# Kernel tuning notes

Measured on AMD Instinct MI355X. Metric: run time of the kernel, lower is better.

The kernel has to match this reference:

```python
import jax, jax.numpy as jnp
import numpy as np

B = 64        # graphs
N0 = 2048     # nodes per graph
DEG = 16      # avg degree
IN = 128      # input_dim
H = 30        # hcs
NH = 11       # heads
OD = 8        # output_dim[i]
K1, K2, K3 = 1844, 1660, 1494  # ceil(0.9*n) chain


def setup_inputs() -> dict:
    key = jax.random.key(0)
    ks = jax.random.split(key, 32)
    N = B * N0
    E = N * DEG
    x = jax.random.normal(ks[0], (N, IN), jnp.float32)
    g = jnp.repeat(jnp.arange(B, dtype=jnp.int32), N0 * DEG)
    src = g * N0 + jax.random.randint(ks[1], (E,), 0, N0, dtype=jnp.int32)
    dst = g * N0 + jax.random.randint(ks[2], (E,), 0, N0, dtype=jnp.int32)
    edge_index = jnp.stack([src, dst])
    edge_attr = jax.random.uniform(ks[3], (E,), jnp.float32)
    batch = jnp.repeat(jnp.arange(B, dtype=jnp.int32), N0)
    s = 0.05
    def W(k, *shape):
        return jax.random.normal(k, shape, jnp.float32) * s
    return {
        'x': x, 'edge_index': edge_index, 'edge_attr': edge_attr, 'batch': batch,
        'ln_g': jnp.ones((IN,), jnp.float32), 'ln_b': jnp.zeros((IN,), jnp.float32),
        'W_rel1': W(ks[4], IN, H), 'b_rel1': W(ks[5], H), 'W_root1': W(ks[6], IN, H),
        'W_rel2': W(ks[7], H, H), 'b_rel2': W(ks[8], H), 'W_root2': W(ks[9], H, H),
        'W_rel3': W(ks[10], H, H), 'b_rel3': W(ks[11], H), 'W_root3': W(ks[12], H, H),
        'pool_w1': W(ks[13], H), 'pool_w2': W(ks[14], H), 'pool_w3': W(ks[15], H),
        'head_W1': W(ks[16], NH, 2 * H, 8 * H), 'head_b1': W(ks[17], NH, 8 * H),
        'head_W2': W(ks[18], NH, 8 * H, 32 * H), 'head_b2': W(ks[19], NH, 32 * H),
        'head_W3': W(ks[20], NH, 32 * H, OD), 'head_b3': W(ks[21], NH, OD),
    }


def _layernorm(x, g, b):
    m = x.mean(-1, keepdims=True)
    v = ((x - m) ** 2).mean(-1, keepdims=True)
    return (x - m) * jax.lax.rsqrt(v + 1e-5) * g + b


def _gconv(x, src, dst, ew, Wr, br, Ws, N):
    # PyG GraphConv: out = lin_rel(sum_j ew*x_j) + lin_root(x)
    agg = jax.ops.segment_sum(x[src] * ew[:, None], dst, num_segments=N)
    return agg @ Wr + br + x @ Ws


def _topk_pool(x, src, dst, ew, w, n, k):
    # score = tanh(x.w/||w||); keep top-k per graph; gate kept nodes by score
    score = jnp.tanh((x @ w) / jnp.linalg.norm(w)).reshape(B, n)
    vals, idx = jax.lax.top_k(score, k)                      # [B,k]
    xg = x.reshape(B, n, -1)
    xk = jnp.take_along_axis(xg, idx[:, :, None], axis=1) * vals[:, :, None]
    x_new = xk.reshape(B * k, -1)
    newidx = jnp.full((B, n), -1, jnp.int32)
    newidx = newidx.at[jnp.arange(B)[:, None], idx].set(
        jnp.broadcast_to(jnp.arange(k, dtype=jnp.int32), (B, k)))
    g = src // n
    ns = newidx[g, src % n]
    nd = newidx[g, dst % n]
    keep = (ns >= 0) & (nd >= 0)
    src_new = jnp.where(keep, g * k + ns, 0)
    dst_new = jnp.where(keep, g * k + nd, 0)
    ew_new = jnp.where(keep, ew, 0.0)
    return x_new, src_new, dst_new, ew_new


def _readout(x, k):
    xg = x.reshape(B, k, -1)
    return jnp.concatenate([xg.max(axis=1), xg.mean(axis=1)], axis=1)  # [B,2H]


def reference(x, edge_index, edge_attr, batch, ln_g, ln_b,
              W_rel1, b_rel1, W_root1, W_rel2, b_rel2, W_root2,
              W_rel3, b_rel3, W_root3, pool_w1, pool_w2, pool_w3,
              head_W1, head_b1, head_W2, head_b2, head_W3, head_b3):
    src, dst = edge_index[0], edge_index[1]
    ew = edge_attr
    h = _layernorm(x, ln_g, ln_b)

    h = jax.nn.relu(_gconv(h, src, dst, ew, W_rel1, b_rel1, W_root1, B * N0))
    h, src, dst, ew = _topk_pool(h, src, dst, ew, pool_w1, N0, K1)
    x1 = _readout(h, K1)

    h = jax.nn.relu(_gconv(h, src, dst, ew, W_rel2, b_rel2, W_root2, B * K1))
    h, src, dst, ew = _topk_pool(h, src, dst, ew, pool_w2, K1, K2)
    x2 = _readout(h, K2)

    h = jax.nn.relu(_gconv(h, src, dst, ew, W_rel3, b_rel3, W_root3, B * K2))
    h, src, dst, ew = _topk_pool(h, src, dst, ew, pool_w3, K2, K3)
    x3 = _readout(h, K3)

    z = jax.nn.relu(x1 + x2 + x3)                                   # [B,60]
    a = jax.nn.relu(jnp.einsum('bd,hdo->hbo', z, head_W1) + head_b1[:, None, :])
    a = jax.nn.relu(jnp.einsum('hbo,hop->hbp', a, head_W2) + head_b2[:, None, :])
    out = jnp.einsum('hbp,hpq->hbq', a, head_W3) + head_b3[:, None, :]
    return out  # [11, B, 8]
```

## Files before the change

kernel.cpp:

```cpp
#include <hip/hip_runtime.h>
#include <hip/hip_bf16.h>

#define B 64
#define N0 2048
#define DEG 16
#define IN_DIM 128
#define H 30
#define NH 11
#define K1 1844
#define K2 1660
#define K3 1494
#define NTOT (B * N0)
#define ETOT (NTOT * DEG)
#define RSTRIDE 32
#define RT 64
#define ESTRIDE1 32768
#define RSEG 16

__global__ __launch_bounds__(256) void k_prep(
    const float* __restrict__ ln_g, const float* __restrict__ ln_b,
    const float* __restrict__ Wrel1, const float* __restrict__ brel1, const float* __restrict__ Wroot1,
    const float* __restrict__ Wrel2, const float* __restrict__ Wroot2,
    const float* __restrict__ Wrel3, const float* __restrict__ Wroot3,
    float* __restrict__ Wc1, float* __restrict__ S1, float* __restrict__ T1,
    float* __restrict__ Wc2, float* __restrict__ Wc3)
{
    int tid = threadIdx.x;
    for (int i = tid; i < IN_DIM * 60; i += 256) {
        int j = i / 60, c = i - j * 60;
        float w = (c < H) ? Wrel1[j * H + c] : Wroot1[j * H + (c - H)];
        Wc1[i] = w * ln_g[j];
    }
    if (tid < 60) {
        int c = tid;
        float s = 0.f, tt = 0.f;
        for (int j = 0; j < IN_DIM; ++j) {
            float w = (c < H) ? Wrel1[j * H + c] : Wroot1[j * H + (c - H)];
            s += w * ln_g[j];
            tt += w * ln_b[j];
        }
        S1[c] = s;
        T1[c] = (c < H) ? tt : tt + brel1[c - H];
    }
    for (int i = tid; i < H * 60; i += 256) {
        int j = i / 60, c = i - j * 60;
        Wc2[i] = (c < H) ? Wrel2[j * H + c] : Wroot2[j * H + (c - H)];
        Wc3[i] = (c < H) ? Wrel3[j * H + c] : Wroot3[j * H + (c - H)];
    }
}

__global__ __launch_bounds__(256) void k_lnproj(
    const float* __restrict__ x, const float* __restrict__ Wc,
    const float* __restrict__ S, const float* __restrict__ T,
    float* __restrict__ rt)
{
    __shared__ float wlds[IN_DIM * 60];
    for (int i = threadIdx.x; i < IN_DIM * 60 / 4; i += 256)
        ((float4*)wlds)[i] = ((const float4*)Wc)[i];
    __syncthreads();
    int lane = threadIdx.x & 63;
    int wid = __builtin_amdgcn_readfirstlane(threadIdx.x >> 6);
    int c = (lane < 60) ? lane : 59;
    float wreg[IN_DIM];
#pragma unroll
    for (int k = 0; k < IN_DIM; ++k) wreg[k] = wlds[k * 60 + c];
    float Sc = S[c], Tc = T[c];
    int outc = (c < 30) ? c : c + 2;
    int rowbase = (blockIdx.x * 4 + wid) * 64;
    for (int rr = 0; rr < 64; ++rr) {
        int row = rowbase + rr;
        const float4* xr4 = (const float4*)(x + (size_t)row * IN_DIM);
        float xa = x[(size_t)row * IN_DIM + lane];
        float xb = x[(size_t)row * IN_DIM + 64 + lane];
        float s1 = xa + xb;
        float s2 = xa * xa + xb * xb;
#pragma unroll
        for (int off = 32; off > 0; off >>= 1) {
            s1 += __shfl_xor(s1, off, 64);
            s2 += __shfl_xor(s2, off, 64);
        }
        float mean = s1 * (1.f / 128.f);
        float var = s2 * (1.f / 128.f) - mean * mean;
        float rstd = 1.0f / sqrtf(var + 1e-5f);
        float acc0 = 0.f, acc1 = 0.f;
#pragma unroll
        for (int q = 0; q < 32; q += 2) {
            float4 xq0 = xr4[q];
            float4 xq1 = xr4[q + 1];
            acc0 = fmaf(xq0.x, wreg[q * 4 + 0], acc0);
            acc1 = fmaf(xq1.x, wreg[q * 4 + 4], acc1);
            acc0 = fmaf(xq0.y, wreg[q * 4 + 1], acc0);
            acc1 = fmaf(xq1.y, wreg[q * 4 + 5], acc1);
            acc0 = fmaf(xq0.z, wreg[q * 4 + 2], acc0);
            acc1 = fmaf(xq1.z, wreg[q * 4 + 6], acc1);
            acc0 = fmaf(xq0.w, wreg[q * 4 + 3], acc0);
            acc1 = fmaf(xq1.w, wreg[q * 4 + 7], acc1);
        }
        float outv = rstd * ((acc0 + acc1) - mean * Sc) + Tc;
        if (lane < 60)
            rt[(size_t)row * RT + outc] = outv;
    }
}

__global__ __launch_bounds__(256) void k_proj30p(
    const float* __restrict__ hbuf, const int* __restrict__ sidx,
    const float* __restrict__ score, const float* __restrict__ Wc,
    const float* __restrict__ brel, float* __restrict__ rt,
    int n_old, int k)
{
    __shared__ float wlds[4][32][16];
    for (int i = threadIdx.x; i < 30 * 64; i += 256) {
        int m = i >> 6, cc = i & 63;
        int cg = cc >> 4, j = cc & 15;
        wlds[cg][m][j] = (j < 15) ? Wc[m * 60 + cg * 15 + j] : 0.f;
    }
    __syncthreads();
    int lane = threadIdx.x & 63, cg = threadIdx.x >> 6;
    int row0 = blockIdx.x * 256 + lane;
    float acc[4][15];
#pragma unroll
    for (int ri = 0; ri < 4; ++ri)
#pragma unroll
        for (int c = 0; c < 15; ++c) acc[ri][c] = 0.f;
    float vals[4];
    const float* hp[4];
#pragma unroll
    for (int ri = 0; ri < 4; ++ri) {
        int row = row0 + ri * 64;
        int g = row / k, j = row - g * k;
        int idx = sidx[g * k + j];
        vals[ri] = score[g * n_old + idx];
        hp[ri] = hbuf + (size_t)(g * n_old + idx) * RSTRIDE;
    }
    for (int mb = 0; mb < 7; ++mb) {
        float4 cur[4];
#pragma unroll
        for (int ri = 0; ri < 4; ++ri) cur[ri] = *(const float4*)(hp[ri] + mb * 4);
#pragma unroll
        for (int kk = 0; kk < 4; ++kk) {
            int m = mb * 4 + kk;
            float4 w0 = *(const float4*)&wlds[cg][m][0];
            float4 w1 = *(const float4*)&wlds[cg][m][4];
            float4 w2 = *(const float4*)&wlds[cg][m][8];
            float4 w3 = *(const float4*)&wlds[cg][m][12];
#pragma unroll
            for (int ri = 0; ri < 4; ++ri) {
                float xv = (kk == 0) ? cur[ri].x : (kk == 1) ? cur[ri].y
                          : (kk == 2) ? cur[ri].z : cur[ri].w;
                acc[ri][0]  += xv * w0.x; acc[ri][1]  += xv * w0.y;
                acc[ri][2]  += xv * w0.z; acc[ri][3]  += xv * w0.w;
                acc[ri][4]  += xv * w1.x; acc[ri][5]  += xv * w1.y;
                acc[ri][6]  += xv * w1.z; acc[ri][7]  += xv * w1.w;
                acc[ri][8]  += xv * w2.x; acc[ri][9]  += xv * w2.y;
                acc[ri][10] += xv * w2.z; acc[ri][11] += xv * w2.w;
                acc[ri][12] += xv * w3.x; acc[ri][13] += xv * w3.y;
                acc[ri][14] += xv * w3.z;
            }
        }
    }
    {
        float2 h2[4];
#pragma unroll
        for (int ri = 0; ri < 4; ++ri) h2[ri] = *(const float2*)(hp[ri] + 28);
#pragma unroll
        for (int kk = 0; kk < 2; ++kk) {
            int m = 28 + kk;
            float4 w0 = *(const float4*)&wlds[cg][m][0];
            float4 w1 = *(const float4*)&wlds[cg][m][4];
            float4 w2 = *(const float4*)&wlds[cg][m][8];
            float4 w3 = *(const float4*)&wlds[cg][m][12];
#pragma unroll
            for (int ri = 0; ri < 4; ++ri) {
                float xv = (kk == 0) ? h2[ri].x : h2[ri].y;
                acc[ri][0]  += xv * w0.x; acc[ri][1]  += xv * w0.y;
                acc[ri][2]  += xv * w0.z; acc[ri][3]  += xv * w0.w;
                acc[ri][4]  += xv * w1.x; acc[ri][5]  += xv * w1.y;
                acc[ri][6]  += xv * w1.z; acc[ri][7]  += xv * w1.w;
                acc[ri][8]  += xv * w2.x; acc[ri][9]  += xv * w2.y;
                acc[ri][10] += xv * w2.z; acc[ri][11] += xv * w2.w;
                acc[ri][12] += xv * w3.x; acc[ri][13] += xv * w3.y;
                acc[ri][14] += xv * w3.z;
            }
        }
    }
    bool isR = (cg < 2);
    int coff = (isR ? 0 : 32) + (cg & 1) * 15;
    float sB[15];
#pragma unroll
    for (int c = 0; c < 15; ++c) sB[c] = isR ? 0.f : brel[(cg & 1) * 15 + c];
#pragma unroll
    for (int ri = 0; ri < 4; ++ri) {
        int row = row0 + ri * 64;
        float val = vals[ri];
        float* op = rt + (size_t)row * RT + coff;
#pragma unroll
        for (int c = 0; c < 15; ++c)
            op[c] = val * acc[ri][c] + sB[c];
    }
}

__global__ __launch_bounds__(1024) void k_hist1(
    const int* __restrict__ dst, unsigned short* __restrict__ rank,
    int* __restrict__ chunkCnt)
{
    __shared__ unsigned int cnt[2048];
    int chunk = blockIdx.x, g = chunk >> 2;
    for (int i = threadIdx.x; i < 2048; i += 1024) cnt[i] = 0;
    __syncthreads();
    int e0 = chunk * 8192;
#pragma unroll
    for (int u = 0; u < 8; ++u) {
        int e = e0 + u * 1024 + threadIdx.x;
        int d = dst[e] - g * N0;
        rank[e] = (unsigned short)atomicAdd(&cnt[d], 1u);
    }
    __syncthreads();
    for (int i = threadIdx.x; i < 2048; i += 1024) chunkCnt[chunk * 2048 + i] = cnt[i];
}

__global__ __launch_bounds__(1024) void k_scan(
    int* __restrict__ chunkCnt, int* __restrict__ runStart, int* __restrict__ runLen)
{
    __shared__ int bufA[2048], bufB[2048];
    int g = blockIdx.x;
    int c0[2], c1[2], c2[2], tt[2];
    for (int h2 = 0; h2 < 2; ++h2) {
        int d = threadIdx.x + h2 * 1024;
        c0[h2] = chunkCnt[(g * 4 + 0) * 2048 + d];
        c1[h2] = chunkCnt[(g * 4 + 1) * 2048 + d];
        c2[h2] = chunkCnt[(g * 4 + 2) * 2048 + d];
        int c3 = chunkCnt[(g * 4 + 3) * 2048 + d];
        tt[h2] = c0[h2] + c1[h2] + c2[h2] + c3;
        bufA[d] = tt[h2];
    }
    __syncthreads();
    int* s_ = bufA; int* d_ = bufB;
    for (int off = 1; off < 2048; off <<= 1) {
        for (int h2 = 0; h2 < 2; ++h2) {
            int d = threadIdx.x + h2 * 1024;
            int v = s_[d];
            if (d >= off) v += s_[d - off];
            d_[d] = v;
        }
        __syncthreads();
        int* tmp = s_; s_ = d_; d_ = tmp;
    }
    for (int h2 = 0; h2 < 2; ++h2) {
        int d = threadIdx.x + h2 * 1024;
        int ex = s_[d] - tt[h2];
        runStart[g * 2048 + d] = ex;
        runLen[g * 2048 + d] = tt[h2];
        chunkCnt[(g * 4 + 0) * 2048 + d] = ex;
        chunkCnt[(g * 4 + 1) * 2048 + d] = ex + c0[h2];
        chunkCnt[(g * 4 + 2) * 2048 + d] = ex + c0[h2] + c1[h2];
        chunkCnt[(g * 4 + 3) * 2048 + d] = ex + c0[h2] + c1[h2] + c2[h2];
    }
}

__global__ __launch_bounds__(1024) void k_scat1(
    const int* __restrict__ src, const int* __restrict__ dst, const float* __restrict__ ew,
    const unsigned short* __restrict__ rank, const int* __restrict__ chunkOff,
    float2* __restrict__ sOut)
{
    int chunk = blockIdx.x, g = chunk >> 2;
    int e0 = chunk * 8192;
#pragma unroll
    for (int u = 0; u < 8; ++u) {
        int e = e0 + u * 1024 + threadIdx.x;
        int d = dst[e] - g * N0;
        int pos = chunkOff[chunk * 2048 + d] + (int)rank[e];
        sOut[(size_t)g * ESTRIDE1 + pos] = make_float2(__int_as_float(src[e]), ew[e]);
    }
}

template<int LVL>
__global__ __launch_bounds__(256) void k_gather(
    const float2* __restrict__ sE, const int* __restrict__ runS, const int* __restrict__ runL,
    const int* __restrict__ ind1, const int* __restrict__ ind2, const int* __restrict__ mapc,
    const float* __restrict__ rt, float* __restrict__ h,
    const float* __restrict__ poolw, float* __restrict__ score,
    int n, int rK, int nblocks)
{
    int b = blockIdx.x;
    int cpx = nblocks >> 3;
    b = (b & 7) * cpx + (b >> 3);
    int slot = threadIdx.x >> 5, j = threadIdx.x & 31;
    int v = b * 8 + slot;
    int g = v / n;
    int local = v - g * n;
    int v1 = local;
    if (LVL >= 2) v1 = ind2[g * K2 + v1];
    if (LVL >= 1) v1 = ind1[g * K1 + v1];
    int s0 = runS[g * 2048 + v1], len = runL[g * 2048 + v1];
    const float2* meta = sE + (size_t)g * ESTRIDE1 + s0;
    int rbase = g * rK;
    float acc = 0.f;
    for (int c = 0; c < len; c += 8) {
        int lim = len - c; if (lim > 8) lim = 8;
        float2 m[8];
#pragma unroll
        for (int u = 0; u < 8; ++u) m[u] = meta[c + (u < lim ? u : 0)];
        int rowv[8]; float wv[8];
#pragma unroll
        for (int u = 0; u < 8; ++u) {
            int srcg = __float_as_int(m[u].x);
            float w = (u < lim) ? m[u].y : 0.f;
            if (LVL == 0) {
                rowv[u] = srcg;
            } else {
                int ss = mapc[srcg];
                rowv[u] = rbase + (ss < 0 ? 0 : ss);
                w = (ss < 0) ? 0.f : w;
            }
            wv[u] = w;
        }
#pragma unroll
        for (int u = 0; u < 8; ++u)
            acc += rt[(size_t)rowv[u] * RT + j] * wv[u];
    }
    float wj = (j < H) ? poolw[j] : 0.f;
    float hval = 0.f;
    if (j < H) {
        hval = fmaxf(acc + rt[(size_t)v * RT + 32 + j], 0.f);
        h[(size_t)v * RSTRIDE + j] = hval;
    }
    float p = hval * wj, q = wj * wj;
#pragma unroll
    for (int off = 16; off > 0; off >>= 1) {
        p += __shfl_xor(p, off, 32);
        q += __shfl_xor(q, off, 32);
    }
    if (j == 0) score[v] = tanhf(p / sqrtf(q));
}

__global__ __launch_bounds__(1024) void k_topk_map(
    const float* __restrict__ score, int* __restrict__ sidx, int* __restrict__ mapc,
    int n, int k, int first)
{
    __shared__ unsigned long long keys[2048];
    __shared__ int inv[2048];
    int g = blockIdx.x;
    for (int i = threadIdx.x; i < 2048; i += 1024) {
        unsigned long long key = ~0ull;
        if (i < n) {
            float s = score[g * n + i];
            if (s == 0.f) s = 0.f;
            unsigned u = __float_as_uint(s);
            unsigned asc = (u & 0x80000000u) ? ~u : (u | 0x80000000u);
            unsigned desc = ~asc;
            key = ((unsigned long long)desc << 32) | (unsigned)i;
        }
        keys[i] = key;
        inv[i] = -1;
    }
    __syncthreads();
    for (int kk = 2; kk <= 2048; kk <<= 1) {
        for (int jj = kk >> 1; jj > 0; jj >>= 1) {
            for (int i = threadIdx.x; i < 2048; i += 1024) {
                int ixj = i ^ jj;
                if (ixj > i) {
                    unsigned long long a = keys[i], bb = keys[ixj];
                    bool up = ((i & kk) == 0);
                    if ((a > bb) == up) { keys[i] = bb; keys[ixj] = a; }
                }
            }
            __syncthreads();
        }
    }
    for (int j = threadIdx.x; j < k; j += 1024) {
        int idx = (int)(keys[j] & 0xffffffffu);
        sidx[g * k + j] = idx;
        inv[idx] = j;
    }
    __syncthreads();
    if (first) {
        for (int v = threadIdx.x; v < N0; v += 1024)
            mapc[g * N0 + v] = inv[v];
    } else {
        for (int v = threadIdx.x; v < N0; v += 1024) {
            int m = mapc[g * N0 + v];
            mapc[g * N0 + v] = (m >= 0) ? inv[m] : -1;
        }
    }
}

__global__ __launch_bounds__(256) void k_rpart(
    const float* __restrict__ hbuf, const int* __restrict__ sidx,
    const float* __restrict__ score, float* __restrict__ pmax, float* __restrict__ psum,
    int n_old, int k)
{
    __shared__ float smax[8][32], ssum[8][32];
    int g = blockIdx.y, seg = blockIdx.x;
    int clen = (k + RSEG - 1) / RSEG;
    int start = seg * clen;
    int end = start + clen; if (end > k) end = k;
    int f = threadIdx.x & 31, rr = threadIdx.x >> 5;
    float mx = -INFINITY, sm = 0.f;
    if (f < H) {
        for (int j = start + rr; j < end; j += 8) {
            int idx = sidx[g * k + j];
            float val = score[g * n_old + idx];
            float v = hbuf[(size_t)(g * n_old + idx) * RSTRIDE + f] * val;
            mx = fmaxf(mx, v);
            sm += v;
        }
    }
    smax[rr][f] = mx; ssum[rr][f] = sm;
    __syncthreads();
    if (rr == 0) {
        for (int q = 1; q < 8; ++q) { mx = fmaxf(mx, smax[q][f]); sm += ssum[q][f]; }
        pmax[(g * RSEG + seg) * 32 + f] = mx;
        psum[(g * RSEG + seg) * 32 + f] = sm;
    }
}

__global__ __launch_bounds__(64) void k_zfin(
    const float* __restrict__ pm1, const float* __restrict__ ps1,
    const float* __restrict__ pm2, const float* __restrict__ ps2,
    const float* __restrict__ pm3, const float* __restrict__ ps3,
    float* __restrict__ z)
{
    int g = blockIdx.x, c = threadIdx.x;
    if (c >= 60) return;
    float v1, v2, v3;
    if (c < H) {
        float m1 = -INFINITY, m2 = -INFINITY, m3 = -INFINITY;
        for (int s = 0; s < RSEG; ++s) {
            m1 = fmaxf(m1, pm1[(g * RSEG + s) * 32 + c]);
            m2 = fmaxf(m2, pm2[(g * RSEG + s) * 32 + c]);
            m3 = fmaxf(m3, pm3[(g * RSEG + s) * 32 + c]);
        }
        v1 = m1; v2 = m2; v3 = m3;
    } else {
        int f = c - H;
        float s1 = 0.f, s2 = 0.f, s3 = 0.f;
        for (int s = 0; s < RSEG; ++s) {
            s1 += ps1[(g * RSEG + s) * 32 + f];
            s2 += ps2[(g * RSEG + s) * 32 + f];
            s3 += ps3[(g * RSEG + s) * 32 + f];
        }
        v1 = s1 / (float)K1; v2 = s2 / (float)K2; v3 = s3 / (float)K3;
    }
    z[g * 60 + c] = fmaxf(v1 + v2 + v3, 0.f);
}

__global__ __launch_bounds__(256) void k_mlp1(
    const float* __restrict__ z, const float* __restrict__ W,
    const float* __restrict__ bias, float* __restrict__ a)
{
    int hb = blockIdx.x, hh = hb >> 6, b = hb & 63;
    __shared__ float zr[60];
    if (threadIdx.x < 60) zr[threadIdx.x] = z[b * 60 + threadIdx.x];
    __syncthreads();
    int o = threadIdx.x;
    if (o < 240) {
        float acc = bias[hh * 240 + o];
        const float* Wp = W + hh * 60 * 240;
#pragma unroll
        for (int d = 0; d < 60; ++d) acc += zr[d] * Wp[d * 240 + o];
        a[(hh * B + b) * 240 + o] = fmaxf(acc, 0.f);
    }
}

__global__ __launch_bounds__(256) void k_mlp2(
    const float* __restrict__ a1, const float* __restrict__ W,
    const float* __restrict__ bias, float* __restrict__ a2)
{
    __shared__ float a1t[64 * 240];
    int hh = blockIdx.x / 15, ct = blockIdx.x % 15;
    const float4* ag = (const float4*)(a1 + (size_t)hh * B * 240);
    for (int i = threadIdx.x; i < 64 * 240 / 4; i += 256)
        ((float4*)a1t)[i] = ag[i];
    __syncthreads();
    int col = threadIdx.x & 63, rg = threadIdx.x >> 6;
    const float* Wp = W + (size_t)hh * 240 * 960 + ct * 64 + col;
    float acc[16];
#pragma unroll
    for (int i = 0; i < 16; ++i) acc[i] = 0.f;
#pragma unroll 4
    for (int o = 0; o < 240; ++o) {
        float w = Wp[(size_t)o * 960];
        const float* ar = &a1t[0];
#pragma unroll
        for (int i = 0; i < 16; ++i)
            acc[i] += w * ar[(rg * 16 + i) * 240 + o];
    }
    float bv = bias[hh * 960 + ct * 64 + col];
#pragma unroll
    for (int i = 0; i < 16; ++i)
        a2[((size_t)hh * B + rg * 16 + i) * 960 + ct * 64 + col] =
            fmaxf(acc[i] + bv, 0.f);
}

__global__ __launch_bounds__(64) void k_mlp3(
    const float* __restrict__ a2, const float* __restrict__ W,
    const float* __restrict__ bias, float* __restrict__ out)
{
    int hb = blockIdx.x, hh = hb >> 6, b = hb & 63;
    __shared__ float ar[960];
    __shared__ float part[64];
    for (int i = threadIdx.x; i < 960; i += 64) ar[i] = a2[(hh * B + b) * 960 + i];
    __syncthreads();
    int q = threadIdx.x & 7, c = threadIdx.x >> 3;
    const float* Wp = W + hh * 960 * 8;
    float acc = 0.f;
    for (int p = c; p < 960; p += 8) acc += ar[p] * Wp[p * 8 + q];
    part[threadIdx.x] = acc;
    __syncthreads();
    if (threadIdx.x < 8) {
        float s = bias[hh * 8 + threadIdx.x];
        for (int cc = 0; cc < 8; ++cc) s += part[cc * 8 + threadIdx.x];
        out[(hh * B + b) * 8 + threadIdx.x] = s;
    }
}

extern "C" void kernel_launch(void* const* d_in, const int* in_sizes, int n_in,
                              void* d_out, int out_size, void* d_ws, size_t ws_size,
                              hipStream_t stream)
{
    const float* x       = (const float*)d_in[0];
    const int*   eidx    = (const int*)d_in[1];
    const int*   src0    = eidx;
    const int*   dst0    = eidx + ETOT;
    const float* ew0     = (const float*)d_in[2];
    const float* ln_g    = (const float*)d_in[4];
    const float* ln_b    = (const float*)d_in[5];
    const float* W_rel1  = (const float*)d_in[6];
    const float* b_rel1  = (const float*)d_in[7];
    const float* W_root1 = (const float*)d_in[8];
    const float* W_rel2  = (const float*)d_in[9];
    const float* b_rel2  = (const float*)d_in[10];
    const float* W_root2 = (const float*)d_in[11];
    const float* W_rel3  = (const float*)d_in[12];
    const float* b_rel3  = (const float*)d_in[13];
    const float* W_root3 = (const float*)d_in[14];
    const float* pool_w1 = (const float*)d_in[15];
    const float* pool_w2 = (const float*)d_in[16];
    const float* pool_w3 = (const float*)d_in[17];
    const float* head_W1 = (const float*)d_in[18];
    const float* head_b1 = (const float*)d_in[19];
    const float* head_W2 = (const float*)d_in[20];
    const float* head_b2 = (const float*)d_in[21];
    const float* head_W3 = (const float*)d_in[22];
    const float* head_b3 = (const float*)d_in[23];

    float* ws     = (float*)d_ws;
    float* rtbuf  = ws;
    float* abuf   = rtbuf + (size_t)NTOT * RT;
    float2* sA    = (float2*)(abuf + (size_t)NTOT * RSTRIDE);
    float* score  = (float*)(sA + (size_t)B * ESTRIDE1);
    int*   sidxA  = (int*)(score + NTOT);
    int*   sidxB  = sidxA + B * K1;
    int*   sidxC  = sidxB + B * K2;
    int*   mapc   = sidxC + B * K3;
    int*   runSA  = mapc + NTOT;
    int*   runLA  = runSA + B * 2048;
    float* pm1    = (float*)(runLA + B * 2048);
    float* ps1    = pm1 + B * RSEG * 32;
    float* pm2    = ps1 + B * RSEG * 32;
    float* ps2    = pm2 + B * RSEG * 32;
    float* pm3    = ps2 + B * RSEG * 32;
    float* ps3    = pm3 + B * RSEG * 32;
    float* zb     = ps3 + B * RSEG * 32;
    float* Wc1    = zb + B * 60;
    float* S1     = Wc1 + IN_DIM * 60;
    float* T1     = S1 + 60;
    float* Wc2    = T1 + 60;
    float* Wc3    = Wc2 + H * 60;
    int* chunkBuf         = (int*)abuf;
    unsigned short* rank  = (unsigned short*)((char*)abuf + (4u << 20));
    float* a1 = rtbuf;
    float* a2 = a1 + NH * B * 240;

    k_prep<<<1, 256, 0, stream>>>(ln_g, ln_b, W_rel1, b_rel1, W_root1,
                                  W_rel2, W_root2, W_rel3, W_root3,
                                  Wc1, S1, T1, Wc2, Wc3);

    k_hist1<<<256, 1024, 0, stream>>>(dst0, rank, chunkBuf);
    k_scan<<<B, 1024, 0, stream>>>(chunkBuf, runSA, runLA);
    k_scat1<<<256, 1024, 0, stream>>>(src0, dst0, ew0, rank, chunkBuf, sA);

    k_lnproj<<<NTOT / 256, 256, 0, stream>>>(x, Wc1, S1, T1, rtbuf);
    k_gather<0><<<NTOT / 8, 256, 0, stream>>>(sA, runSA, runLA, nullptr, nullptr, nullptr,
                                              rtbuf, abuf, pool_w1, score,
                                              N0, N0, NTOT / 8);
    k_topk_map<<<B, 1024, 0, stream>>>(score, sidxA, mapc, N0, K1, 1);
    k_rpart<<<dim3(RSEG, B), 256, 0, stream>>>(abuf, sidxA, score, pm1, ps1, N0, K1);
    k_proj30p<<<B * K1 / 256, 256, 0, stream>>>(abuf, sidxA, score, Wc2, b_rel2,
                                                rtbuf, N0, K1);

    k_gather<1><<<B * K1 / 8, 256, 0, stream>>>(sA, runSA, runLA, sidxA, nullptr, mapc,
                                                rtbuf, abuf, pool_w2, score,
                                                K1, K1, B * K1 / 8);
    k_topk_map<<<B, 1024, 0, stream>>>(score, sidxB, mapc, K1, K2, 0);
    k_rpart<<<dim3(RSEG, B), 256, 0, stream>>>(abuf, sidxB, score, pm2, ps2, K1, K2);
    k_proj30p<<<B * K2 / 256, 256, 0, stream>>>(abuf, sidxB, score, Wc3, b_rel3,
                                                rtbuf, K1, K2);

    k_gather<2><<<B * K2 / 8, 256, 0, stream>>>(sA, runSA, runLA, sidxA, sidxB, mapc,
                                                rtbuf, abuf, pool_w3, score,
                                                K2, K2, B * K2 / 8);
    k_topk_map<<<B, 1024, 0, stream>>>(score, sidxC, mapc, K2, K3, 0);
    k_rpart<<<dim3(RSEG, B), 256, 0, stream>>>(abuf, sidxC, score, pm3, ps3, K2, K3);

    k_zfin<<<B, 64, 0, stream>>>(pm1, ps1, pm2, ps2, pm3, ps3, zb);
    k_mlp1<<<NH * B, 256, 0, stream>>>(zb, head_W1, head_b1, a1);
    k_mlp2<<<NH * 15, 256, 0, stream>>>(a1, head_W2, head_b2, a2);
    k_mlp3<<<NH * B, 64, 0, stream>>>(a2, head_W3, head_b3, (float*)d_out);
}
```

Measured before the change: 568.0 us.

## Remap projection kernels to thread-per-row with column groups on grid y

Rewrites k_lnproj and k_proj30p so that each thread computes one row for a 15-column group, with the group chosen by blockIdx.y. Weights are read directly from global memory with uniform addresses instead of being staged in LDS or held in 128 registers per lane. The goal is to cut register and LDS pressure and raise occupancy. The cost is that each input row is now read four times, and the per-thread row reads are strided rather than coalesced across a wave.

Result: slower. 674.0 us (+18.7%).

```diff
diff --git a/kernel.cpp b/kernel.cpp
--- a/kernel.cpp
+++ b/kernel.cpp
@@ -54,52 +54,35 @@
     const float* __restrict__ S, const float* __restrict__ T,
     float* __restrict__ rt)
 {
-    __shared__ float wlds[IN_DIM * 60];
-    for (int i = threadIdx.x; i < IN_DIM * 60 / 4; i += 256)
-        ((float4*)wlds)[i] = ((const float4*)Wc)[i];
-    __syncthreads();
-    int lane = threadIdx.x & 63;
-    int wid = __builtin_amdgcn_readfirstlane(threadIdx.x >> 6);
-    int c = (lane < 60) ? lane : 59;
-    float wreg[IN_DIM];
-#pragma unroll
-    for (int k = 0; k < IN_DIM; ++k) wreg[k] = wlds[k * 60 + c];
-    float Sc = S[c], Tc = T[c];
-    int outc = (c < 30) ? c : c + 2;
-    int rowbase = (blockIdx.x * 4 + wid) * 64;
-    for (int rr = 0; rr < 64; ++rr) {
-        int row = rowbase + rr;
-        const float4* xr4 = (const float4*)(x + (size_t)row * IN_DIM);
-        float xa = x[(size_t)row * IN_DIM + lane];
-        float xb = x[(size_t)row * IN_DIM + 64 + lane];
-        float s1 = xa + xb;
-        float s2 = xa * xa + xb * xb;
-#pragma unroll
-        for (int off = 32; off > 0; off >>= 1) {
-            s1 += __shfl_xor(s1, off, 64);
-            s2 += __shfl_xor(s2, off, 64);
-        }
-        float mean = s1 * (1.f / 128.f);
-        float var = s2 * (1.f / 128.f) - mean * mean;
-        float rstd = 1.0f / sqrtf(var + 1e-5f);
-        float acc0 = 0.f, acc1 = 0.f;
-#pragma unroll
-        for (int q = 0; q < 32; q += 2) {
-            float4 xq0 = xr4[q];
-            float4 xq1 = xr4[q + 1];
-            acc0 = fmaf(xq0.x, wreg[q * 4 + 0], acc0);
-            acc1 = fmaf(xq1.x, wreg[q * 4 + 4], acc1);
-            acc0 = fmaf(xq0.y, wreg[q * 4 + 1], acc0);
-            acc1 = fmaf(xq1.y, wreg[q * 4 + 5], acc1);
-            acc0 = fmaf(xq0.z, wreg[q * 4 + 2], acc0);
-            acc1 = fmaf(xq1.z, wreg[q * 4 + 6], acc1);
-            acc0 = fmaf(xq0.w, wreg[q * 4 + 3], acc0);
-            acc1 = fmaf(xq1.w, wreg[q * 4 + 7], acc1);
-        }
-        float outv = rstd * ((acc0 + acc1) - mean * Sc) + Tc;
-        if (lane < 60)
-            rt[(size_t)row * RT + outc] = outv;
-    }
+    int cg = blockIdx.y;
+    int row = blockIdx.x * 256 + threadIdx.x;
+    const float4* xr4 = (const float4*)(x + (size_t)row * IN_DIM);
+    const float* wbase = Wc + cg * 15;
+    float acc[15];
+#pragma unroll
+    for (int c = 0; c < 15; ++c) acc[c] = 0.f;
+    float sum = 0.f, sumsq = 0.f;
+    for (int k4 = 0; k4 < 32; ++k4) {
+        float4 xq = xr4[k4];
+        float xs[4] = {xq.x, xq.y, xq.z, xq.w};
+#pragma unroll
+        for (int u = 0; u < 4; ++u) {
+            float xv = xs[u];
+            sum += xv; sumsq += xv * xv;
+            const float* wrow = wbase + (k4 * 4 + u) * 60;
+#pragma unroll
+            for (int c = 0; c < 15; ++c) acc[c] += xv * wrow[c];
+        }
+    }
+    float mean = sum * (1.f / 128.f);
+    float var = sumsq * (1.f / 128.f) - mean * mean;
+    float rstd = 1.0f / sqrtf(var + 1e-5f);
+    int scol = cg * 15;
+    int coff = (cg < 2) ? cg * 15 : 32 + (cg - 2) * 15;
+    float* op = rt + (size_t)row * RT + coff;
+#pragma unroll
+    for (int c = 0; c < 15; ++c)
+        op[c] = rstd * (acc[c] - mean * S[scol + c]) + T[scol + c];
 }
 
 __global__ __launch_bounds__(256) void k_proj30p(
@@ -108,94 +91,44 @@
     const float* __restrict__ brel, float* __restrict__ rt,
     int n_old, int k)
 {
-    __shared__ float wlds[4][32][16];
-    for (int i = threadIdx.x; i < 30 * 64; i += 256) {
-        int m = i >> 6, cc = i & 63;
-        int cg = cc >> 4, j = cc & 15;
-        wlds[cg][m][j] = (j < 15) ? Wc[m * 60 + cg * 15 + j] : 0.f;
-    }
-    __syncthreads();
-    int lane = threadIdx.x & 63, cg = threadIdx.x >> 6;
-    int row0 = blockIdx.x * 256 + lane;
-    float acc[4][15];
-#pragma unroll
-    for (int ri = 0; ri < 4; ++ri)
-#pragma unroll
-        for (int c = 0; c < 15; ++c) acc[ri][c] = 0.f;
-    float vals[4];
-    const float* hp[4];
-#pragma unroll
-    for (int ri = 0; ri < 4; ++ri) {
-        int row = row0 + ri * 64;
-        int g = row / k, j = row - g * k;
-        int idx = sidx[g * k + j];
-        vals[ri] = score[g * n_old + idx];
-        hp[ri] = hbuf + (size_t)(g * n_old + idx) * RSTRIDE;
-    }
-    for (int mb = 0; mb < 7; ++mb) {
-        float4 cur[4];
-#pragma unroll
-        for (int ri = 0; ri < 4; ++ri) cur[ri] = *(const float4*)(hp[ri] + mb * 4);
-#pragma unroll
-        for (int kk = 0; kk < 4; ++kk) {
-            int m = mb * 4 + kk;
-            float4 w0 = *(const float4*)&wlds[cg][m][0];
-            float4 w1 = *(const float4*)&wlds[cg][m][4];
-            float4 w2 = *(const float4*)&wlds[cg][m][8];
-            float4 w3 = *(const float4*)&wlds[cg][m][12];
-#pragma unroll
-            for (int ri = 0; ri < 4; ++ri) {
-                float xv = (kk == 0) ? cur[ri].x : (kk == 1) ? cur[ri].y
-                          : (kk == 2) ? cur[ri].z : cur[ri].w;
-                acc[ri][0]  += xv * w0.x; acc[ri][1]  += xv * w0.y;
-                acc[ri][2]  += xv * w0.z; acc[ri][3]  += xv * w0.w;
-                acc[ri][4]  += xv * w1.x; acc[ri][5]  += xv * w1.y;
-                acc[ri][6]  += xv * w1.z; acc[ri][7]  += xv * w1.w;
-                acc[ri][8]  += xv * w2.x; acc[ri][9]  += xv * w2.y;
-                acc[ri][10] += xv * w2.z; acc[ri][11] += xv * w2.w;
-                acc[ri][12] += xv * w3.x; acc[ri][13] += xv * w3.y;
-                acc[ri][14] += xv * w3.z;
-            }
+    int cg = blockIdx.y;
+    int row = blockIdx.x * 256 + threadIdx.x;
+    int g = row / k, j = row - g * k;
+    int idx = sidx[g * k + j];
+    float val = score[g * n_old + idx];
+    const float* hr = hbuf + (size_t)(g * n_old + idx) * RSTRIDE;
+    const float4* hr4 = (const float4*)hr;
+    const float* wbase = Wc + cg * 15;
+    float acc[15];
+#pragma unroll
+    for (int c = 0; c < 15; ++c) acc[c] = 0.f;
+#pragma unroll
+    for (int m4 = 0; m4 < 7; ++m4) {
+        float4 hq = hr4[m4];
+        float xs[4] = {hq.x, hq.y, hq.z, hq.w};
+#pragma unroll
+        for (int u = 0; u < 4; ++u) {
+            float xv = xs[u];
+            const float* wrow = wbase + (m4 * 4 + u) * 60;
+#pragma unroll
+            for (int c = 0; c < 15; ++c) acc[c] += xv * wrow[c];
         }
     }
     {
-        float2 h2[4];
-#pragma unroll
-        for (int ri = 0; ri < 4; ++ri) h2[ri] = *(const float2*)(hp[ri] + 28);
-#pragma unroll
-        for (int kk = 0; kk < 2; ++kk) {
-            int m = 28 + kk;
-            float4 w0 = *(const float4*)&wlds[cg][m][0];
-            float4 w1 = *(const float4*)&wlds[cg][m][4];
-            float4 w2 = *(const float4*)&wlds[cg][m][8];
-            float4 w3 = *(const float4*)&wlds[cg][m][12];
-#pragma unroll
-            for (int ri = 0; ri < 4; ++ri) {
-                float xv = (kk == 0) ? h2[ri].x : h2[ri].y;
-                acc[ri][0]  += xv * w0.x; acc[ri][1]  += xv * w0.y;
-                acc[ri][2]  += xv * w0.z; acc[ri][3]  += xv * w0.w;
-                acc[ri][4]  += xv * w1.x; acc[ri][5]  += xv * w1.y;
-                acc[ri][6]  += xv * w1.z; acc[ri][7]  += xv * w1.w;
-                acc[ri][8]  += xv * w2.x; acc[ri][9]  += xv * w2.y;
-                acc[ri][10] += xv * w2.z; acc[ri][11] += xv * w2.w;
-                acc[ri][12] += xv * w3.x; acc[ri][13] += xv * w3.y;
-                acc[ri][14] += xv * w3.z;
-            }
-        }
+        float2 h2 = *(const float2*)(hr + 28);
+        const float* w28 = wbase + 28 * 60;
+        const float* w29 = wbase + 29 * 60;
+#pragma unroll
+        for (int c = 0; c < 15; ++c)
+            acc[c] += h2.x * w28[c] + h2.y * w29[c];
     }
     bool isR = (cg < 2);
-    int coff = (isR ? 0 : 32) + (cg & 1) * 15;
-    float sB[15];
-#pragma unroll
-    for (int c = 0; c < 15; ++c) sB[c] = isR ? 0.f : brel[(cg & 1) * 15 + c];
-#pragma unroll
-    for (int ri = 0; ri < 4; ++ri) {
-        int row = row0 + ri * 64;
-        float val = vals[ri];
-        float* op = rt + (size_t)row * RT + coff;
-#pragma unroll
-        for (int c = 0; c < 15; ++c)
-            op[c] = val * acc[ri][c] + sB[c];
+    int coff = isR ? cg * 15 : 32 + (cg - 2) * 15;
+    float* op = rt + (size_t)row * RT + coff;
+#pragma unroll
+    for (int c = 0; c < 15; ++c) {
+        float bv = isR ? 0.f : brel[(cg - 2) * 15 + c];
+        op[c] = val * acc[c] + bv;
     }
 }
 
@@ -580,22 +513,22 @@
     k_scan<<<B, 1024, 0, stream>>>(chunkBuf, runSA, runLA);
     k_scat1<<<256, 1024, 0, stream>>>(src0, dst0, ew0, rank, chunkBuf, sA);
 
-    k_lnproj<<<NTOT / 256, 256, 0, stream>>>(x, Wc1, S1, T1, rtbuf);
+    k_lnproj<<<dim3(NTOT / 256, 4), 256, 0, stream>>>(x, Wc1, S1, T1, rtbuf);
     k_gather<0><<<NTOT / 8, 256, 0, stream>>>(sA, runSA, runLA, nullptr, nullptr, nullptr,
                                               rtbuf, abuf, pool_w1, score,
                                               N0, N0, NTOT / 8);
     k_topk_map<<<B, 1024, 0, stream>>>(score, sidxA, mapc, N0, K1, 1);
     k_rpart<<<dim3(RSEG, B), 256, 0, stream>>>(abuf, sidxA, score, pm1, ps1, N0, K1);
-    k_proj30p<<<B * K1 / 256, 256, 0, stream>>>(abuf, sidxA, score, Wc2, b_rel2,
-                                                rtbuf, N0, K1);
+    k_proj30p<<<dim3(B * K1 / 256, 4), 256, 0, stream>>>(abuf, sidxA, score, Wc2, b_rel2,
+                                                         rtbuf, N0, K1);
 
     k_gather<1><<<B * K1 / 8, 256, 0, stream>>>(sA, runSA, runLA, sidxA, nullptr, mapc,
                                                 rtbuf, abuf, pool_w2, score,
                                                 K1, K1, B * K1 / 8);
     k_topk_map<<<B, 1024, 0, stream>>>(score, sidxB, mapc, K1, K2, 0);
     k_rpart<<<dim3(RSEG, B), 256, 0, stream>>>(abuf, sidxB, score, pm2, ps2, K1, K2);
-    k_proj30p<<<B * K2 / 256, 256, 0, stream>>>(abuf, sidxB, score, Wc3, b_rel3,
-                                                rtbuf, K1, K2);
+    k_proj30p<<<dim3(B * K2 / 256, 4), 256, 0, stream>>>(abuf, sidxB, score, Wc3, b_rel3,
+                                                         rtbuf, K1, K2);
 
     k_gather<2><<<B * K2 / 8, 256, 0, stream>>>(sA, runSA, runLA, sidxA, sidxB, mapc,
                                                 rtbuf, abuf, pool_w3, score,
```
